# Kernel tuning notes

Hardware: AMD Instinct MI355X
Metric: run time of the kernel (lower is better)

Reference implementation:

```python
import jax, jax.numpy as jnp
import numpy as np

B, N, F = 8, 500000, 1000000


def setup_inputs() -> dict:
    key = jax.random.key(0)
    k1, k2 = jax.random.split(key)
    vert = jax.random.normal(k1, (B, N, 3), dtype=jnp.float32)
    faces = jax.random.randint(k2, (F, 3), 0, N, dtype=jnp.int64)
    return {"vert": vert, "faces": faces}


def _uniform_laplacian(vert, faces):
    # vert: [B, N, 3], faces: [F, 3]
    n = vert.shape[1]
    i, j, k = faces[:, 0], faces[:, 1], faces[:, 2]
    # 6 directed edges per face: dst accumulates its neighbors' positions (src)
    dst = jnp.concatenate([i, i, j, j, k, k])  # [6F]
    src = jnp.concatenate([j, k, i, k, i, j])  # [6F]
    deg = jax.ops.segment_sum(jnp.ones_like(dst, dtype=vert.dtype), dst, num_segments=n)  # [N]
    nbr_sum = jax.vmap(lambda v: jax.ops.segment_sum(v[src], dst, num_segments=n))(vert)  # [B,N,3]
    # lap = mean(neighbors) - v  (uniform Laplacian: D^{-1} A - I)
    return nbr_sum / jnp.maximum(deg, 1.0)[None, :, None] - vert


def reference(vert, faces):
    lap = _uniform_laplacian(vert, faces)          # [B, N, 3]
    curve = jnp.sqrt(jnp.sum(lap * lap, axis=-1))  # [B, N] (L2 norm over xyz)
    return curve
```

## Files before the change

kernel.cpp:

```cpp
#include <hip/hip_runtime.h>
#include <hip/hip_fp16.h>
#include <math.h>

#define BATCH 8
#define NBUK_MAX 512
#define BSHIFT 10
#define CAPB 6656
#define PACK_MASK 0x7FFFFull
#define EXP_T 512
#define FACES_PER_BLOCK 1024
#define STAGE_SZ (FACES_PER_BLOCK * 3)
#define SCAN_T 256
#define SCAN_E 8
#define SCAN_TILE (SCAN_T * SCAN_E)

union H2U { __half2 h; unsigned u; };

__device__ __forceinline__ long long pack3(int v, int a, int b) {
    return (long long)(((unsigned long long)(unsigned)v) |
                       ((unsigned long long)(unsigned)a << 19) |
                       ((unsigned long long)(unsigned)b << 38));
}

__global__ __launch_bounds__(EXP_T, 8) void expand_repack_kernel(
        const int* __restrict__ faces,
        int* __restrict__ cursor,
        long long* __restrict__ recbuf,
        const float* __restrict__ vert,
        uint2* __restrict__ vh,
        int N, int F, int expBlocks) {
    if ((int)blockIdx.x < expBlocks) {
        __shared__ int hist[NBUK_MAX];
        __shared__ int lbase[NBUK_MAX];
        __shared__ int gb[NBUK_MAX];
        __shared__ int wsum[8];
        __shared__ int s_total;
        __shared__ long long stage[STAGE_SZ];
        int tid = threadIdx.x;
        hist[tid] = 0;
        __syncthreads();

        int fbase = blockIdx.x * FACES_PER_BLOCK;
        int f0 = fbase + tid;
        int f1 = fbase + EXP_T + tid;
        bool val0 = f0 < F;
        bool val1 = f1 < F;

        int i0 = 0, j0 = 0, k0 = 0, i1 = 0, j1 = 0, k1 = 0;
        if (val0) { i0 = faces[3 * f0 + 0]; j0 = faces[3 * f0 + 1]; k0 = faces[3 * f0 + 2]; }
        if (val1) { i1 = faces[3 * f1 + 0]; j1 = faces[3 * f1 + 1]; k1 = faces[3 * f1 + 2]; }

        int bb0 = 0, bb1 = 0, bb2 = 0, bb3 = 0, bb4 = 0, bb5 = 0;
        int rr0 = 0, rr1 = 0, rr2 = 0, rr3 = 0, rr4 = 0, rr5 = 0;
        long long rc0 = 0, rc1 = 0, rc2 = 0, rc3 = 0, rc4 = 0, rc5 = 0;
        if (val0) {
            rc0 = pack3(i0, j0, k0);
            rc1 = pack3(j0, i0, k0);
            rc2 = pack3(k0, i0, j0);
            bb0 = i0 >> BSHIFT; bb1 = j0 >> BSHIFT; bb2 = k0 >> BSHIFT;
            rr0 = atomicAdd(&hist[bb0], 1);
            rr1 = atomicAdd(&hist[bb1], 1);
            rr2 = atomicAdd(&hist[bb2], 1);
        }
        if (val1) {
            rc3 = pack3(i1, j1, k1);
            rc4 = pack3(j1, i1, k1);
            rc5 = pack3(k1, i1, j1);
            bb3 = i1 >> BSHIFT; bb4 = j1 >> BSHIFT; bb5 = k1 >> BSHIFT;
            rr3 = atomicAdd(&hist[bb3], 1);
            rr4 = atomicAdd(&hist[bb4], 1);
            rr5 = atomicAdd(&hist[bb5], 1);
        }
        __syncthreads();

        int lane = tid & 63;
        int wv = tid >> 6;
        int h = hist[tid];
        int incl = h;
        #pragma unroll
        for (int d = 1; d < 64; d <<= 1) {
            int t = __shfl_up(incl, d, 64);
            if (lane >= d) incl += t;
        }
        if (lane == 63) wsum[wv] = incl;
        __syncthreads();
        int pre = 0;
        #pragma unroll
        for (int w = 0; w < 8; ++w)
            pre += (w < wv) ? wsum[w] : 0;
        incl += pre;
        lbase[tid] = incl - h;
        gb[tid] = (h > 0) ? atomicAdd(&cursor[tid * 16], h) : 0;
        if (tid == NBUK_MAX - 1) s_total = incl;
        __syncthreads();

        if (val0) {
            stage[lbase[bb0] + rr0] = rc0;
            stage[lbase[bb1] + rr1] = rc1;
            stage[lbase[bb2] + rr2] = rc2;
        }
        if (val1) {
            stage[lbase[bb3] + rr3] = rc3;
            stage[lbase[bb4] + rr4] = rc4;
            stage[lbase[bb5] + rr5] = rc5;
        }
        __syncthreads();

        int total = s_total;
        for (int t = tid; t < total; t += EXP_T) {
            long long r = stage[t];
            int v = (int)((unsigned long long)r & PACK_MASK);
            int b = v >> BSHIFT;
            int gpos = gb[b] + (t - lbase[b]);
            if (gpos < CAPB)
                recbuf[(size_t)b * CAPB + gpos] = r;
        }
    } else {
        int u = (blockIdx.x - expBlocks) * EXP_T + threadIdx.x;
        if (u < N * BATCH) {
            int v = u >> 3;
            int b = u & 7;
            size_t src = ((size_t)b * N + v) * 3;
            H2U xy, zw;
            xy.h = __floats2half2_rn(vert[src], vert[src + 1]);
            zw.h = __floats2half2_rn(vert[src + 2], 0.0f);
            uint2 w; w.x = xy.u; w.y = zw.u;
            vh[u] = w;
        }
    }
}

__device__ __forceinline__ void unpack_acc(uint2 r, float& ax, float& ay, float& az) {
    H2U xy, zw; xy.u = r.x; zw.u = r.y;
    float2 f0 = __half22float2(xy.h);
    float2 f1 = __half22float2(zw.h);
    ax += f0.x; ay += f0.y; az += f1.x;
}

__global__ __launch_bounds__(1024) void bucket_gather_kernel(
        const int* __restrict__ cursor,
        const long long* __restrict__ recbuf,
        const uint2* __restrict__ vh,
        float* __restrict__ out, int N) {
    __shared__ int cntL[1024];
    __shared__ int offL[1024];
    __shared__ int2 colbuf[CAPB];
    int tid = threadIdx.x;
    int bid = blockIdx.x;
    int v0 = bid << BSHIFT;

    int rc = cursor[bid * 16];
    int rcnt = rc < CAPB ? rc : CAPB;

    cntL[tid] = 0;
    __syncthreads();
    const long long* recs = recbuf + (size_t)bid * CAPB;
    for (int x = tid; x < rcnt; x += 1024) {
        int v = (int)((unsigned long long)recs[x] & PACK_MASK);
        atomicAdd(&cntL[v & 1023], 2);
    }
    __syncthreads();

    int myc = cntL[tid];
    for (int d = 1; d < 1024; d <<= 1) {
        int t = (tid >= d) ? cntL[tid - d] : 0;
        __syncthreads();
        cntL[tid] += t;
        __syncthreads();
    }
    int myoff = cntL[tid] - myc;
    cntL[tid] = myoff;
    offL[tid] = myoff;
    __syncthreads();

    for (int x = tid; x < rcnt; x += 1024) {
        unsigned long long r = (unsigned long long)recs[x];
        int v = (int)(r & PACK_MASK);
        int a = (int)((r >> 19) & PACK_MASK);
        int b = (int)((r >> 38) & PACK_MASK);
        int p = atomicAdd(&cntL[v & 1023], 2);
        colbuf[p >> 1] = make_int2(a, b);
    }
    __syncthreads();

    int b = tid & 7;
    for (int it = 0; it < (1 << BSHIFT) / 128; ++it) {
        int lv = (tid >> 3) + 128 * it;
        int v = v0 + lv;
        if (v >= N) continue;
        int start = offL[lv];
        int end = cntL[lv];
        int c = end - start;
        int e = start >> 1, e1 = end >> 1;

        float ax = 0.f, ay = 0.f, az = 0.f;
        for (; e + 4 <= e1; e += 4) {
            int2 s01 = colbuf[e];
            int2 s23 = colbuf[e + 1];
            int2 s45 = colbuf[e + 2];
            int2 s67 = colbuf[e + 3];
            uint2 r0 = vh[((size_t)s01.x << 3) + b];
            uint2 r1 = vh[((size_t)s01.y << 3) + b];
            uint2 r2 = vh[((size_t)s23.x << 3) + b];
            uint2 r3 = vh[((size_t)s23.y << 3) + b];
            uint2 r4 = vh[((size_t)s45.x << 3) + b];
            uint2 r5 = vh[((size_t)s45.y << 3) + b];
            uint2 r6 = vh[((size_t)s67.x << 3) + b];
            uint2 r7 = vh[((size_t)s67.y << 3) + b];
            unpack_acc(r0, ax, ay, az); unpack_acc(r1, ax, ay, az);
            unpack_acc(r2, ax, ay, az); unpack_acc(r3, ax, ay, az);
            unpack_acc(r4, ax, ay, az); unpack_acc(r5, ax, ay, az);
            unpack_acc(r6, ax, ay, az); unpack_acc(r7, ax, ay, az);
        }
        for (; e < e1; ++e) {
            int2 ss = colbuf[e];
            uint2 r0 = vh[((size_t)ss.x << 3) + b];
            uint2 r1 = vh[((size_t)ss.y << 3) + b];
            unpack_acc(r0, ax, ay, az);
            unpack_acc(r1, ax, ay, az);
        }

        float invd = 1.0f / fmaxf((float)c, 1.0f);
        float sx = 0.f, sy = 0.f, sz = 0.f;
        unpack_acc(vh[((size_t)v << 3) + b], sx, sy, sz);
        float l0 = ax * invd - sx;
        float l1 = ay * invd - sy;
        float l2 = az * invd - sz;
        out[(size_t)b * N + v] = sqrtf(l0 * l0 + l1 * l1 + l2 * l2);
    }
}


__global__ void count_only_kernel(const int* __restrict__ faces, int* __restrict__ cnt,
                                  int* __restrict__ rank, int F) {
    int f = blockIdx.x * blockDim.x + threadIdx.x;
    if (f >= F) return;
    rank[3 * f + 0] = atomicAdd(&cnt[faces[3 * f + 0]], 2);
    rank[3 * f + 1] = atomicAdd(&cnt[faces[3 * f + 1]], 2);
    rank[3 * f + 2] = atomicAdd(&cnt[faces[3 * f + 2]], 2);
}

__global__ void scan_sums_kernel(const int* __restrict__ cnt, int* __restrict__ bsums, int N) {
    __shared__ int sh[SCAN_T];
    int base = blockIdx.x * SCAN_TILE + threadIdx.x * SCAN_E;
    int s = 0;
    #pragma unroll
    for (int e = 0; e < SCAN_E; ++e)
        if (base + e < N) s += cnt[base + e];
    sh[threadIdx.x] = s;
    __syncthreads();
    for (int d = SCAN_T / 2; d > 0; d >>= 1) {
        if (threadIdx.x < (unsigned)d) sh[threadIdx.x] += sh[threadIdx.x + d];
        __syncthreads();
    }
    if (threadIdx.x == 0) bsums[blockIdx.x] = sh[0];
}

__global__ void scan_apply_kernel(const int* __restrict__ cnt, int* __restrict__ off,
                                  const int* __restrict__ bsums, int N, int nb) {
    __shared__ int shb[SCAN_T];
    __shared__ int sh[SCAN_T];
    int bv = ((int)threadIdx.x < nb) ? bsums[threadIdx.x] : 0;
    shb[threadIdx.x] = bv;
    __syncthreads();
    for (int d = 1; d < SCAN_T; d <<= 1) {
        int t = (threadIdx.x >= (unsigned)d) ? shb[threadIdx.x - d] : 0;
        __syncthreads();
        shb[threadIdx.x] += t;
        __syncthreads();
    }
    int block_prefix = (blockIdx.x > 0) ? shb[blockIdx.x - 1] : 0;

    int base = blockIdx.x * SCAN_TILE + threadIdx.x * SCAN_E;
    int vals[SCAN_E];
    int s = 0;
    #pragma unroll
    for (int e = 0; e < SCAN_E; ++e) {
        int v = (base + e < N) ? cnt[base + e] : 0;
        vals[e] = v; s += v;
    }
    sh[threadIdx.x] = s;
    __syncthreads();
    for (int d = 1; d < SCAN_T; d <<= 1) {
        int t = (threadIdx.x >= (unsigned)d) ? sh[threadIdx.x - d] : 0;
        __syncthreads();
        sh[threadIdx.x] += t;
        __syncthreads();
    }
    int excl = block_prefix + ((threadIdx.x > 0) ? sh[threadIdx.x - 1] : 0);
    #pragma unroll
    for (int e = 0; e < SCAN_E; ++e) {
        if (base + e < N) off[base + e] = excl;
        excl += vals[e];
    }
}

__global__ void fill_kernel(const int* __restrict__ faces, const int* __restrict__ off,
                            const int* __restrict__ rank, int* __restrict__ col, int F) {
    int f = blockIdx.x * blockDim.x + threadIdx.x;
    if (f >= F) return;
    int i = faces[3 * f + 0];
    int j = faces[3 * f + 1];
    int k = faces[3 * f + 2];
    int2* c2 = (int2*)col;
    c2[(off[i] + rank[3 * f + 0]) >> 1] = make_int2(j, k);
    c2[(off[j] + rank[3 * f + 1]) >> 1] = make_int2(i, k);
    c2[(off[k] + rank[3 * f + 2]) >> 1] = make_int2(i, j);
}

__global__ void gather_scalar_kernel(const float* __restrict__ vert,
                                     const int* __restrict__ cnt,
                                     const int* __restrict__ off,
                                     const int* __restrict__ col,
                                     float* __restrict__ out, int N) {
    int v = blockIdx.x * blockDim.x + threadIdx.x;
    if (v >= N) return;
    int c = cnt[v];
    int start = off[v];
    int end = start + c;
    float ax[BATCH], ay[BATCH], az[BATCH];
    #pragma unroll
    for (int b = 0; b < BATCH; ++b) { ax[b] = 0.f; ay[b] = 0.f; az[b] = 0.f; }
    for (int e = start; e < end; ++e) {
        int s = col[e];
        #pragma unroll
        for (int b = 0; b < BATCH; ++b) {
            size_t base = ((size_t)b * N + s) * 3;
            ax[b] += vert[base + 0];
            ay[b] += vert[base + 1];
            az[b] += vert[base + 2];
        }
    }
    float invd = 1.0f / fmaxf((float)c, 1.0f);
    #pragma unroll
    for (int b = 0; b < BATCH; ++b) {
        size_t base = ((size_t)b * N + v) * 3;
        float l0 = ax[b] * invd - vert[base + 0];
        float l1 = ay[b] * invd - vert[base + 1];
        float l2 = az[b] * invd - vert[base + 2];
        out[(size_t)b * N + v] = sqrtf(l0 * l0 + l1 * l1 + l2 * l2);
    }
}


static inline size_t align256(size_t x) { return (x + 255) & ~(size_t)255; }

extern "C" void kernel_launch(void* const* d_in, const int* in_sizes, int n_in,
                              void* d_out, int out_size, void* d_ws, size_t ws_size,
                              hipStream_t stream) {
    const float* vert  = (const float*)d_in[0];
    const int*   faces = (const int*)d_in[1];
    float*       out   = (float*)d_out;

    int N = out_size / BATCH;
    int F = in_sizes[1] / 3;
    int E = 6 * F;
    int NB = (N + (1 << BSHIFT) - 1) >> BSHIFT;

    char* ws = (char*)d_ws;

    size_t o_cursor = 0;
    size_t o_vh     = NBUK_MAX * 64;
    size_t o_rec    = o_vh + align256((size_t)N * BATCH * sizeof(uint2));
    size_t need     = o_rec + (size_t)NB * CAPB * 8;

    if (ws_size >= need && N <= 524288 && NB <= NBUK_MAX) {
        int*       cursor = (int*)(ws + o_cursor);
        uint2*     vh     = (uint2*)(ws + o_vh);
        long long* rec    = (long long*)(ws + o_rec);

        (void)hipMemsetAsync(cursor, 0, NBUK_MAX * 64, stream);

        int expB = (F + FACES_PER_BLOCK - 1) / FACES_PER_BLOCK;
        int repB = (N * BATCH + EXP_T - 1) / EXP_T;
        expand_repack_kernel<<<expB + repB, EXP_T, 0, stream>>>(
            faces, cursor, rec, vert, vh, N, F, expB);

        bucket_gather_kernel<<<NB, 1024, 0, stream>>>(cursor, rec, vh, out, N);
        return;
    }

    int threads = 256;
    int nb = (N + SCAN_TILE - 1) / SCAN_TILE;
    size_t f_cnt   = 0;
    size_t f_off   = align256((size_t)N * 4);
    size_t f_bsums = f_off + align256((size_t)N * 4);
    size_t f_col   = f_bsums + 4096;
    size_t f_rank  = f_col + align256((size_t)E * 4);

    int* cnt   = (int*)(ws + f_cnt);
    int* off   = (int*)(ws + f_off);
    int* bsums = (int*)(ws + f_bsums);
    int* col   = (int*)(ws + f_col);
    int* rank  = (int*)(ws + f_rank);

    (void)hipMemsetAsync(cnt, 0, (size_t)N * 4, stream);

    int cntBlocks = (F + threads - 1) / threads;
    count_only_kernel<<<cntBlocks, threads, 0, stream>>>(faces, cnt, rank, F);
    scan_sums_kernel<<<nb, SCAN_T, 0, stream>>>(cnt, bsums, N);
    scan_apply_kernel<<<nb, SCAN_T, 0, stream>>>(cnt, off, bsums, N, nb);
    fill_kernel<<<cntBlocks, threads, 0, stream>>>(faces, off, rank, col, F);
    gather_scalar_kernel<<<(N + threads - 1) / threads, threads, 0, stream>>>(
        vert, cnt, off, col, out, N);
}
```

Measured before the change: 235.9 us.

## Coalesce vertex repack via LDS transpose, enlarge expand blocks, stagger bucket atomics

The half-precision repack path now loads 128 vertices across all 8 batches with contiguous reads into shared memory. It then transposes them so each thread writes one batch-interleaved uint2. Before, each thread read strided float triples. The expand path doubles to 1024 threads and 2048 faces per block, and rotates the order in which buckets issue their global cursor atomics per block to spread contention. The larger stage buffer and block size raise LDS use and lower the number of resident blocks. The scan now uses barriers inside a tid-split branch, which relies on both sides reaching the same barrier count.

```diff
diff --git a/kernel.cpp b/kernel.cpp
--- a/kernel.cpp
+++ b/kernel.cpp
@@ -7,9 +7,10 @@
 #define BSHIFT 10
 #define CAPB 6656
 #define PACK_MASK 0x7FFFFull
-#define EXP_T 512
-#define FACES_PER_BLOCK 1024
+#define EXP_T 1024
+#define FACES_PER_BLOCK 2048
 #define STAGE_SZ (FACES_PER_BLOCK * 3)
+#define REPACK_V 128
 #define SCAN_T 256
 #define SCAN_E 8
 #define SCAN_TILE (SCAN_T * SCAN_E)
@@ -22,22 +23,23 @@
                        ((unsigned long long)(unsigned)b << 38));
 }
 
-__global__ __launch_bounds__(EXP_T, 8) void expand_repack_kernel(
+__global__ __launch_bounds__(EXP_T) void expand_repack_kernel(
         const int* __restrict__ faces,
         int* __restrict__ cursor,
         long long* __restrict__ recbuf,
         const float* __restrict__ vert,
         uint2* __restrict__ vh,
         int N, int F, int expBlocks) {
+    __shared__ int hist[NBUK_MAX];
+    __shared__ int lbase[NBUK_MAX];
+    __shared__ int gb[NBUK_MAX];
+    __shared__ int wsum[8];
+    __shared__ int s_total;
+    __shared__ long long stage[STAGE_SZ];
+    int tid = threadIdx.x;
+
     if ((int)blockIdx.x < expBlocks) {
-        __shared__ int hist[NBUK_MAX];
-        __shared__ int lbase[NBUK_MAX];
-        __shared__ int gb[NBUK_MAX];
-        __shared__ int wsum[8];
-        __shared__ int s_total;
-        __shared__ long long stage[STAGE_SZ];
-        int tid = threadIdx.x;
-        hist[tid] = 0;
+        if (tid < NBUK_MAX) hist[tid] = 0;
         __syncthreads();
 
         int fbase = blockIdx.x * FACES_PER_BLOCK;
@@ -73,25 +75,31 @@
         }
         __syncthreads();
 
-        int lane = tid & 63;
-        int wv = tid >> 6;
-        int h = hist[tid];
-        int incl = h;
-        #pragma unroll
-        for (int d = 1; d < 64; d <<= 1) {
-            int t = __shfl_up(incl, d, 64);
-            if (lane >= d) incl += t;
-        }
-        if (lane == 63) wsum[wv] = incl;
-        __syncthreads();
-        int pre = 0;
-        #pragma unroll
-        for (int w = 0; w < 8; ++w)
-            pre += (w < wv) ? wsum[w] : 0;
-        incl += pre;
-        lbase[tid] = incl - h;
-        gb[tid] = (h > 0) ? atomicAdd(&cursor[tid * 16], h) : 0;
-        if (tid == NBUK_MAX - 1) s_total = incl;
+        if (tid < NBUK_MAX) {
+            int lane = tid & 63;
+            int wv = tid >> 6;
+            int h = hist[tid];
+            int incl = h;
+            #pragma unroll
+            for (int d = 1; d < 64; d <<= 1) {
+                int t = __shfl_up(incl, d, 64);
+                if (lane >= d) incl += t;
+            }
+            if (lane == 63) wsum[wv] = incl;
+            __syncthreads();
+            int pre = 0;
+            #pragma unroll
+            for (int w = 0; w < 8; ++w)
+                pre += (w < wv) ? wsum[w] : 0;
+            incl += pre;
+            lbase[tid] = incl - h;
+            if (tid == NBUK_MAX - 1) s_total = incl;
+            int rb = (tid + (int)blockIdx.x * 197) & (NBUK_MAX - 1);
+            int hrb = hist[rb];
+            gb[rb] = (hrb > 0) ? atomicAdd(&cursor[rb * 16], hrb) : 0;
+        } else {
+            __syncthreads();
+        }
         __syncthreads();
 
         if (val0) {
@@ -116,16 +124,30 @@
                 recbuf[(size_t)b * CAPB + gpos] = r;
         }
     } else {
-        int u = (blockIdx.x - expBlocks) * EXP_T + threadIdx.x;
-        if (u < N * BATCH) {
-            int v = u >> 3;
-            int b = u & 7;
-            size_t src = ((size_t)b * N + v) * 3;
+        float* lf = (float*)stage;
+        int v0 = (blockIdx.x - expBlocks) * REPACK_V;
+        int vlim = N - v0; if (vlim > REPACK_V) vlim = REPACK_V;
+        int flim = 3 * vlim;
+        #pragma unroll
+        for (int p = 0; p < 3; ++p) {
+            int L = tid + p * 1024;
+            int b = L >> 8; b = L / 384;
+            int off = L - b * 384;
+            if (off < flim)
+                lf[off * 9 + b] = vert[((size_t)b * N + v0) * 3 + off];
+        }
+        __syncthreads();
+        int lv = tid >> 3;
+        int b = tid & 7;
+        if (lv < vlim) {
+            float x = lf[(3 * lv + 0) * 9 + b];
+            float y = lf[(3 * lv + 1) * 9 + b];
+            float z = lf[(3 * lv + 2) * 9 + b];
             H2U xy, zw;
-            xy.h = __floats2half2_rn(vert[src], vert[src + 1]);
-            zw.h = __floats2half2_rn(vert[src + 2], 0.0f);
+            xy.h = __floats2half2_rn(x, y);
+            zw.h = __floats2half2_rn(z, 0.0f);
             uint2 w; w.x = xy.u; w.y = zw.u;
-            vh[u] = w;
+            vh[((size_t)(v0 + lv) << 3) + b] = w;
         }
     }
 }
@@ -372,7 +394,7 @@
         (void)hipMemsetAsync(cursor, 0, NBUK_MAX * 64, stream);
 
         int expB = (F + FACES_PER_BLOCK - 1) / FACES_PER_BLOCK;
-        int repB = (N * BATCH + EXP_T - 1) / EXP_T;
+        int repB = (N + REPACK_V - 1) / REPACK_V;
         expand_repack_kernel<<<expB + repB, EXP_T, 0, stream>>>(
             faces, cursor, rec, vert, vh, N, F, expB);
 
```

Result: faster. 230.2 us (-2.4%).
